# Kernel optimization log

Measured on AMD Instinct MI355X. Metric: run time of the kernel, lower is better.

The kernel has to match this reference:

```python
import jax, jax.numpy as jnp
import numpy as np

EPS = 1e-5

def setup_inputs() -> dict:
    key = jax.random.key(0)
    ks = jax.random.split(key, 4)
    B, C, H, W = 32, 256, 32, 32
    x = jax.random.normal(ks[0], (B, C, H, W), dtype=jnp.float32)
    gamma = jnp.ones((C,), dtype=jnp.float32)
    beta = jnp.zeros((C,), dtype=jnp.float32)
    # torch nn.Linear init scale ~ 1/sqrt(fan_in)
    W_kqv = jax.random.normal(ks[1], (3 * C, C), dtype=jnp.float32) / np.sqrt(C)
    b_kqv = jnp.zeros((3 * C,), dtype=jnp.float32)
    W_proj = jax.random.normal(ks[2], (C, C), dtype=jnp.float32) / np.sqrt(C)
    b_proj = jnp.zeros((C,), dtype=jnp.float32)
    return {"x": x, "gamma": gamma, "beta": beta, "W_kqv": W_kqv,
            "b_kqv": b_kqv, "W_proj": W_proj, "b_proj": b_proj}

def reference(x, gamma, beta, W_kqv, b_kqv, W_proj, b_proj):
    B, C, H, W = x.shape
    scale = jnp.sqrt(jnp.asarray(C, dtype=x.dtype))
    # BatchNorm2d (training-mode batch statistics, biased variance, eps=1e-5)
    mean = jnp.mean(x, axis=(0, 2, 3), keepdims=True)
    var = jnp.var(x, axis=(0, 2, 3), keepdims=True)
    t = (x - mean) * jax.lax.rsqrt(var + EPS)
    t = t * gamma[None, :, None, None] + beta[None, :, None, None]
    # [B, C, H, W] -> [B, N, C] with N = H*W
    t = t.reshape(B, C, H * W).transpose(0, 2, 1)
    kqv = t @ W_kqv.T + b_kqv           # [B, N, 3C]
    q, k, v = jnp.split(kqv, 3, axis=-1)  # each [B, N, C]
    s = jnp.einsum('bnc,bmc->bnm', q, k) / scale  # [B, N, N]
    attn = jax.nn.softmax(s, axis=-1)
    o = jnp.einsum('bnm,bmc->bnc', attn, v)        # [B, N, C]
    o = o @ W_proj.T + b_proj
    o = o.transpose(0, 2, 1).reshape(B, C, H, W)
    return o + x
```

## Files before the change

kernel.cpp:

```cpp
#include <hip/hip_runtime.h>

typedef unsigned short u16;
typedef __attribute__((ext_vector_type(8))) short bf16x8;
typedef __attribute__((ext_vector_type(4))) float f32x4;

__device__ __forceinline__ float bf2f(u16 u) {
  union { unsigned u; float f; } c; c.u = ((unsigned)u) << 16; return c.f;
}
__device__ __forceinline__ u16 f2bf(float f) {
  union { float f; unsigned u; } c; c.f = f;
  unsigned u = c.u;
  return (u16)((u + 0x7FFFu + ((u >> 16) & 1u)) >> 16);
}
__device__ __forceinline__ void gld16(const void* g, void* l) {
  __builtin_amdgcn_global_load_lds(
      (__attribute__((address_space(1))) void*)g,
      (__attribute__((address_space(3))) void*)l, 16, 0, 0);
}

#define SYNCB() do { \
  asm volatile("s_waitcnt vmcnt(0) lgkmcnt(0)" ::: "memory"); \
  __builtin_amdgcn_s_barrier(); \
  __builtin_amdgcn_sched_barrier(0); \
} while (0)

#define BB 32
#define CC 256
#define NN 1024

__global__ __launch_bounds__(256) void convert_w_kernel(
    const float* __restrict__ Wk, const float* __restrict__ bk,
    const float* __restrict__ Wp, const float* __restrict__ bp,
    u16* __restrict__ Wkb, u16* __restrict__ bkb,
    u16* __restrict__ Wpb, u16* __restrict__ bpb)
{
  int b = blockIdx.x, t = threadIdx.x;
  const float* src; u16* dst; int idx, n;
  if (b < 768)       { src = Wk; dst = Wkb; idx = b * 256 + t;        n = 196608; }
  else if (b < 771)  { src = bk; dst = bkb; idx = (b - 768) * 256 + t; n = 768;   }
  else if (b < 1027) { src = Wp; dst = Wpb; idx = (b - 771) * 256 + t; n = 65536; }
  else               { src = bp; dst = bpb; idx = t;                  n = 256;    }
  if (idx < n) dst[idx] = f2bf(src[idx]);
}

__global__ __launch_bounds__(256) void bn_stats_kernel(
    const float* __restrict__ x, const float* __restrict__ gamma,
    const float* __restrict__ beta, float* __restrict__ scl, float* __restrict__ sft)
{
  int c = blockIdx.x;
  int tid = threadIdx.x;
  float s = 0.f, q = 0.f;
  for (int g = tid; g < 8192; g += 256) {
    int b = g >> 8;
    int n = (g & 255) * 4;
    float4 v = *reinterpret_cast<const float4*>(x + (((size_t)(b * CC + c)) << 10) + n);
    s += v.x + v.y + v.z + v.w;
    q += v.x * v.x + v.y * v.y + v.z * v.z + v.w * v.w;
  }
  __shared__ float rs[256], rq[256];
  rs[tid] = s; rq[tid] = q;
  __syncthreads();
  for (int off = 128; off > 0; off >>= 1) {
    if (tid < off) { rs[tid] += rs[tid + off]; rq[tid] += rq[tid + off]; }
    __syncthreads();
  }
  if (tid == 0) {
    float mean = rs[0] * (1.f / 32768.f);
    float var  = rq[0] * (1.f / 32768.f) - mean * mean;
    float rstd = rsqrtf(var + 1e-5f);
    float g = gamma[c] * rstd;
    scl[c] = g;
    sft[c] = beta[c] - mean * g;
  }
}

__global__ __launch_bounds__(256, 2) void qkv_fused_kernel(
    const float* __restrict__ x, const float* __restrict__ scl,
    const float* __restrict__ sft, const u16* __restrict__ Wkb,
    const u16* __restrict__ bkb, u16* __restrict__ qkout, u16* __restrict__ vt)
{
  __shared__ __align__(16) u16 As[2][128 * 32];
  __shared__ __align__(16) u16 Bs[2][256 * 32];
  __shared__ __align__(16) float SS[512];
  int bid = blockIdx.x;
  int bx = bid & 255, by = bid >> 8;
  int b = bx >> 3, nsp0 = (bx & 7) * 128;
  int tid = threadIdx.x, lane = tid & 63, w = tid >> 6;
  int lq = lane & 15, quad = lane >> 4;
  int wm = (w >> 1) * 64, wn = (w & 1) * 128;
  int ar = lane >> 2, ac = (lane & 3) * 8;
  int rbB = w * 64;
  int nn = tid & 127, ci0 = (tid >> 7) * 16;

  const float* xb = x + (((size_t)(b * CC)) << 10) + nsp0 + nn;
  const u16* Bw = Wkb + (size_t)(by * 256) * 256;

  f32x4 zero = {0.f, 0.f, 0.f, 0.f};
  f32x4 acc[4][8];
  #pragma unroll
  for (int i = 0; i < 4; ++i)
    #pragma unroll
    for (int j = 0; j < 8; ++j) acc[i][j] = zero;

  int swz = (nn >> 1) & 3;
  int jj0 = ci0 >> 3;

  if (tid < 128) {
    const float* src = (tid < 64) ? (scl + tid * 4) : (sft + (tid - 64) * 4);
    float4 v = *reinterpret_cast<const float4*>(src);
    *reinterpret_cast<float4*>(&SS[(tid < 64) ? tid * 4 : 256 + (tid - 64) * 4]) = v;
  }
  __syncthreads();

  float xA[16], xB[16];
  #pragma unroll
  for (int i = 0; i < 4; ++i)
    gld16(Bw + (size_t)(rbB + i * 16 + ar) * 256 + ac, &Bs[0][(rbB + i * 16) * 32]);
  #pragma unroll
  for (int i = 0; i < 16; ++i)
    xA[i] = xb[((size_t)(ci0 + i)) << 10];

  auto body = [&](int t, float (&xc)[16], float (&xn)[16]) {
    int k0 = t * 32;
    if (t < 7) {
      int kn = k0 + 32;
      #pragma unroll
      for (int i = 0; i < 4; ++i)
        gld16(Bw + (size_t)(rbB + i * 16 + ar) * 256 + kn + ac,
              &Bs[(t + 1) & 1][(rbB + i * 16) * 32]);
      #pragma unroll
      for (int i = 0; i < 16; ++i)
        xn[i] = xb[((size_t)(kn + ci0 + i)) << 10];
    }
    float sv[16], hv[16];
    #pragma unroll
    for (int g = 0; g < 4; ++g) {
      f32x4 a = *reinterpret_cast<const f32x4*>(&SS[k0 + ci0 + g * 4]);
      f32x4 d = *reinterpret_cast<const f32x4*>(&SS[256 + k0 + ci0 + g * 4]);
      sv[g * 4 + 0] = a[0]; sv[g * 4 + 1] = a[1]; sv[g * 4 + 2] = a[2]; sv[g * 4 + 3] = a[3];
      hv[g * 4 + 0] = d[0]; hv[g * 4 + 1] = d[1]; hv[g * 4 + 2] = d[2]; hv[g * 4 + 3] = d[3];
    }
    if (t < 7) {
      asm volatile("s_waitcnt vmcnt(20)" ::: "memory");
    } else {
      asm volatile("s_waitcnt vmcnt(0)" ::: "memory");
    }
    __builtin_amdgcn_sched_barrier(0);
    u16 av[16];
    #pragma unroll
    for (int i = 0; i < 16; ++i)
      av[i] = f2bf(xc[i] * sv[i] + hv[i]);
    bf16x8 p0, p1;
    #pragma unroll
    for (int i = 0; i < 8; ++i) { p0[i] = (short)av[i]; p1[i] = (short)av[i + 8]; }
    *reinterpret_cast<bf16x8*>(&As[t & 1][nn * 32 + ((jj0 ^ swz) << 3)]) = p0;
    *reinterpret_cast<bf16x8*>(&As[t & 1][nn * 32 + (((jj0 + 1) ^ swz) << 3)]) = p1;
    asm volatile("s_waitcnt lgkmcnt(0)" ::: "memory");
    __builtin_amdgcn_s_barrier();
    __builtin_amdgcn_sched_barrier(0);

    bf16x8 af[4], bfr[8];
    #pragma unroll
    for (int i = 0; i < 4; ++i) {
      int r = wm + i * 16 + lq;
      af[i] = *reinterpret_cast<const bf16x8*>(
          &As[t & 1][r * 32 + ((quad ^ ((r >> 1) & 3)) << 3)]);
    }
    #pragma unroll
    for (int j = 0; j < 8; ++j)
      bfr[j] = *reinterpret_cast<const bf16x8*>(
          &Bs[t & 1][(wn + j * 16 + lq) * 32 + quad * 8]);
    __builtin_amdgcn_s_setprio(1);
    #pragma unroll
    for (int i = 0; i < 4; ++i)
      #pragma unroll
      for (int j = 0; j < 8; ++j)
        acc[i][j] = __builtin_amdgcn_mfma_f32_16x16x32_bf16(af[i], bfr[j], acc[i][j], 0, 0, 0);
    __builtin_amdgcn_s_setprio(0);
    asm volatile("s_waitcnt lgkmcnt(0)" ::: "memory");
    __builtin_amdgcn_s_barrier();
    __builtin_amdgcn_sched_barrier(0);
  };

  #pragma unroll 1
  for (int tt = 0; tt < 4; ++tt) {
    body(2 * tt,     xA, xB);
    body(2 * tt + 1, xB, xA);
  }

  if (by < 2) {
    #pragma unroll
    for (int j = 0; j < 8; ++j) {
      int col = by * 256 + wn + j * 16 + lq;
      float bv = bf2f(bkb[col]);
      #pragma unroll
      for (int i = 0; i < 4; ++i) {
        int m = (b << 10) + nsp0 + wm + i * 16 + quad * 4;
        #pragma unroll
        for (int r = 0; r < 4; ++r)
          qkout[(size_t)(m + r) * 512 + col] = f2bf(acc[i][j][r] + bv);
      }
    }
  } else {
    #pragma unroll
    for (int j = 0; j < 8; ++j) {
      int col = wn + j * 16 + lq;
      float bv = bf2f(bkb[512 + col]);
      #pragma unroll
      for (int i = 0; i < 4; ++i) {
        int n = nsp0 + wm + i * 16 + quad * 4;
        ushort4 o;
        o.x = f2bf(acc[i][j][0] + bv);
        o.y = f2bf(acc[i][j][1] + bv);
        o.z = f2bf(acc[i][j][2] + bv);
        o.w = f2bf(acc[i][j][3] + bv);
        *reinterpret_cast<ushort4*>(&vt[(size_t)b * 262144 + (size_t)col * 1024 + n]) = o;
      }
    }
  }
}

__global__ __launch_bounds__(256) void gemm_nt_kernel(
    const u16* __restrict__ A, int lda, size_t sA,
    const u16* __restrict__ B, int ldb, size_t sB,
    u16* __restrict__ C, int ldc, size_t sC,
    int K, const u16* __restrict__ bias, float scale, int mode,
    const float* __restrict__ xres, float* __restrict__ outf)
{
  __shared__ u16 As[128 * 32];
  __shared__ u16 Bs[128 * 32];
  int tid = threadIdx.x;
  int m0 = blockIdx.x * 128, n0 = blockIdx.y * 128;
  const u16* Ab = A + (size_t)blockIdx.z * sA;
  const u16* Bb = B + (size_t)blockIdx.z * sB;
  u16* Cb = C + (size_t)blockIdx.z * sC;

  int lane = tid & 63, w = tid >> 6;
  int lq = lane & 15, quad = lane >> 4;
  int wm = (w >> 1) * 64, wn = (w & 1) * 64;
  int ar = lane >> 2, ac = (lane & 3) * 8;
  int rb = w * 32;

  f32x4 zero = {0.f, 0.f, 0.f, 0.f};
  f32x4 acc[4][4];
  #pragma unroll
  for (int i = 0; i < 4; ++i)
    #pragma unroll
    for (int j = 0; j < 4; ++j) acc[i][j] = zero;

  for (int k0 = 0; k0 < K; k0 += 32) {
    __syncthreads();
    gld16(Ab + (size_t)(m0 + rb +      ar) * lda + k0 + ac, &As[(rb     ) * 32]);
    gld16(Ab + (size_t)(m0 + rb + 16 + ar) * lda + k0 + ac, &As[(rb + 16) * 32]);
    gld16(Bb + (size_t)(n0 + rb +      ar) * ldb + k0 + ac, &Bs[(rb     ) * 32]);
    gld16(Bb + (size_t)(n0 + rb + 16 + ar) * ldb + k0 + ac, &Bs[(rb + 16) * 32]);
    __syncthreads();
    bf16x8 af[4], bfr[4];
    #pragma unroll
    for (int i = 0; i < 4; ++i) {
      af[i]  = *reinterpret_cast<const bf16x8*>(&As[(wm + i * 16 + lq) * 32 + quad * 8]);
      bfr[i] = *reinterpret_cast<const bf16x8*>(&Bs[(wn + i * 16 + lq) * 32 + quad * 8]);
    }
    #pragma unroll
    for (int i = 0; i < 4; ++i)
      #pragma unroll
      for (int j = 0; j < 4; ++j)
        acc[i][j] = __builtin_amdgcn_mfma_f32_16x16x32_bf16(af[i], bfr[j], acc[i][j], 0, 0, 0);
  }

  #pragma unroll
  for (int j = 0; j < 4; ++j) {
    int col = n0 + wn + j * 16 + lq;
    float bv = bias ? bf2f(bias[col]) : 0.f;
    #pragma unroll
    for (int i = 0; i < 4; ++i) {
      int rbase = m0 + wm + i * 16 + quad * 4;
      if (mode == 2) {
        int b = rbase >> 10, n = rbase & 1023;
        size_t idx = (((size_t)(b * CC + col)) << 10) + n;
        float4 xv = *reinterpret_cast<const float4*>(xres + idx);
        float4 o;
        o.x = acc[i][j][0] * scale + bv + xv.x;
        o.y = acc[i][j][1] * scale + bv + xv.y;
        o.z = acc[i][j][2] * scale + bv + xv.z;
        o.w = acc[i][j][3] * scale + bv + xv.w;
        *reinterpret_cast<float4*>(outf + idx) = o;
      } else {
        #pragma unroll
        for (int r = 0; r < 4; ++r)
          Cb[(size_t)(rbase + r) * ldc + col] = f2bf(acc[i][j][r] * scale + bv);
      }
    }
  }
}

__global__ __launch_bounds__(512, 2) void attn_kernel(
    const u16* __restrict__ qk,
    const u16* __restrict__ vt,
    u16* __restrict__ o)
{
  __shared__ __align__(16) u16 Ks[2][64 * 256];
  __shared__ __align__(16) u16 Vs[2][256 * 64];
  __shared__ __align__(16) u16 Ps[128 * 64];
  float* rs = (float*)Ps;

  int bid = blockIdx.x;
  int b  = (bid & 7) + 8 * ((bid >> 3) & 3);
  int qt = bid >> 5;
  int tid = threadIdx.x, lane = tid & 63, w = tid >> 6;
  int lq = lane & 15, hh = lane >> 4;
  int wr = w & 3;
  bool isQK = w < 4;

  const u16* qb = qk + ((size_t)b << 10) * 512;
  const u16* kb = qb + 256;
  const u16* vb = vt + ((size_t)b << 18);

  auto stageK = [&](int kt, int bufi) {
    #pragma unroll
    for (int i = 0; i < 4; ++i) {
      int slot = i * 512 + tid;
      int r = slot >> 5, c = slot & 31;
      gld16(kb + (size_t)(kt * 64 + r) * 512 + ((c ^ (r & 7)) << 3),
            &Ks[bufi][(i * 512 + (tid & 448)) * 8]);
    }
  };
  auto stageV = [&](int kt, int bufi) {
    #pragma unroll
    for (int i = 0; i < 4; ++i) {
      int slot = i * 512 + tid;
      int n = slot >> 3, c = slot & 7;
      gld16(vb + (size_t)(n << 10) + kt * 64 + ((c ^ (n & 7)) << 3),
            &Vs[bufi][(i * 512 + (tid & 448)) * 8]);
    }
  };

  f32x4 zero = {0.f, 0.f, 0.f, 0.f};

  stageK(0, 0);
  SYNCB();

  if (isQK) {
    int q0 = qt * 128 + wr * 32;
    bf16x8 qf[2][8];
    #pragma unroll
    for (int qi = 0; qi < 2; ++qi)
      #pragma unroll
      for (int kk = 0; kk < 8; ++kk)
        qf[qi][kk] = *reinterpret_cast<const bf16x8*>(
            qb + (size_t)(q0 + qi * 16 + lq) * 512 + kk * 32 + hh * 8);
    float runsum[2][4] = {{0.f, 0.f, 0.f, 0.f}, {0.f, 0.f, 0.f, 0.f}};

    #pragma unroll 1
    for (int p = 0; p <= 16; ++p) {
      if (p <= 15) stageV(p, p & 1);
      if (p <= 14) stageK(p + 1, (p + 1) & 1);
      u16 pbv[2][4][4];
      if (p <= 15) {
        const u16* Kc = Ks[p & 1];
        f32x4 sacc[2][4];
        #pragma unroll
        for (int qi = 0; qi < 2; ++qi)
          #pragma unroll
          for (int ni = 0; ni < 4; ++ni) sacc[qi][ni] = zero;
        #pragma unroll
        for (int kk = 0; kk < 8; ++kk) {
          bf16x8 kf[4];
          #pragma unroll
          for (int ni = 0; ni < 4; ++ni) {
            int r = ni * 16 + lq;
            kf[ni] = *reinterpret_cast<const bf16x8*>(
                &Kc[r * 256 + (((kk * 4 + hh) ^ (r & 7)) << 3)]);
          }
          __builtin_amdgcn_s_setprio(1);
          #pragma unroll
          for (int qi = 0; qi < 2; ++qi)
            #pragma unroll
            for (int ni = 0; ni < 4; ++ni)
              sacc[qi][ni] = __builtin_amdgcn_mfma_f32_16x16x32_bf16(
                  qf[qi][kk], kf[ni], sacc[qi][ni], 0, 0, 0);
          __builtin_amdgcn_s_setprio(0);
        }
        #pragma unroll
        for (int qi = 0; qi < 2; ++qi)
          #pragma unroll
          for (int ni = 0; ni < 4; ++ni)
            #pragma unroll
            for (int rr = 0; rr < 4; ++rr) {
              float pexp = __expf(sacc[qi][ni][rr] * 0.0625f);
              u16 pb = f2bf(pexp);
              runsum[qi][rr] += bf2f(pb);
              pbv[qi][ni][rr] = pb;
            }
      }
      SYNCB();
      if (p <= 15) {
        #pragma unroll
        for (int qi = 0; qi < 2; ++qi)
          #pragma unroll
          for (int ni = 0; ni < 4; ++ni)
            #pragma unroll
            for (int rr = 0; rr < 4; ++rr) {
              int q = wr * 32 + qi * 16 + hh * 4 + rr;
              int kcol = ni * 16 + lq;
              Ps[q * 64 + ((((kcol >> 3) ^ (q & 7)) << 3) | (kcol & 7))] =
                  pbv[qi][ni][rr];
            }
      }
      SYNCB();
    }

    #pragma unroll
    for (int qi = 0; qi < 2; ++qi)
      #pragma unroll
      for (int rr = 0; rr < 4; ++rr) {
        float s = runsum[qi][rr];
        s += __shfl_xor(s, 1, 64);
        s += __shfl_xor(s, 2, 64);
        s += __shfl_xor(s, 4, 64);
        s += __shfl_xor(s, 8, 64);
        if (lq == 0) rs[wr * 32 + qi * 16 + hh * 4 + rr] = 1.f / s;
      }
    SYNCB();
  } else {
    f32x4 oacc[8][4];
    #pragma unroll
    for (int qi = 0; qi < 8; ++qi)
      #pragma unroll
      for (int nj = 0; nj < 4; ++nj) oacc[qi][nj] = zero;

    #pragma unroll 1
    for (int p = 0; p <= 16; ++p) {
      if (p <= 15) stageV(p, p & 1);
      if (p <= 14) stageK(p + 1, (p + 1) & 1);
      if (p >= 1) {
        const u16* Vc = Vs[(p - 1) & 1];
        #pragma unroll
        for (int kk2 = 0; kk2 < 2; ++kk2) {
          bf16x8 pa[8];
          #pragma unroll
          for (int qi = 0; qi < 8; ++qi) {
            int r = qi * 16 + lq;
            pa[qi] = *reinterpret_cast<const bf16x8*>(
                &Ps[r * 64 + (((kk2 * 4 + hh) ^ (r & 7)) << 3)]);
          }
          bf16x8 vf[4];
          #pragma unroll
          for (int nj = 0; nj < 4; ++nj) {
            int n = wr * 64 + nj * 16 + lq;
            vf[nj] = *reinterpret_cast<const bf16x8*>(
                &Vc[n * 64 + (((kk2 * 4 + hh) ^ (n & 7)) << 3)]);
          }
          __builtin_amdgcn_s_setprio(1);
          #pragma unroll
          for (int qi = 0; qi < 8; ++qi)
            #pragma unroll
            for (int nj = 0; nj < 4; ++nj)
              oacc[qi][nj] = __builtin_amdgcn_mfma_f32_16x16x32_bf16(
                  pa[qi], vf[nj], oacc[qi][nj], 0, 0, 0);
          __builtin_amdgcn_s_setprio(0);
        }
      }
      SYNCB();
      SYNCB();
    }

    SYNCB();
    float rinv[8][4];
    #pragma unroll
    for (int qi = 0; qi < 8; ++qi)
      #pragma unroll
      for (int rr = 0; rr < 4; ++rr)
        rinv[qi][rr] = rs[qi * 16 + hh * 4 + rr];
    u16* ob = o + ((size_t)(b << 10) + qt * 128) * 256;
    #pragma unroll
    for (int qi = 0; qi < 8; ++qi)
      #pragma unroll
      for (int nj = 0; nj < 4; ++nj)
        #pragma unroll
        for (int rr = 0; rr < 4; ++rr)
          ob[(size_t)(qi * 16 + hh * 4 + rr) * 256 + wr * 64 + nj * 16 + lq] =
              f2bf(oacc[qi][nj][rr] * rinv[qi][rr]);
  }
}

extern "C" void kernel_launch(void* const* d_in, const int* in_sizes, int n_in,
                              void* d_out, int out_size, void* d_ws, size_t ws_size,
                              hipStream_t stream) {
  const float* x     = (const float*)d_in[0];
  const float* gamma = (const float*)d_in[1];
  const float* beta  = (const float*)d_in[2];
  const float* Wkqv  = (const float*)d_in[3];
  const float* bkqv  = (const float*)d_in[4];
  const float* Wproj = (const float*)d_in[5];
  const float* bproj = (const float*)d_in[6];
  float* out = (float*)d_out;

  char* ws = (char*)d_ws;
  float* scl    = (float*)ws;
  float* sft    = (float*)(ws + 1024);
  u16* Wkb = (u16*)(ws + 4096);
  u16* bkb = Wkb + 196608;
  u16* Wpb = bkb + 768;
  u16* bpb = Wpb + 65536;
  u16* qk   = (u16*)(ws + 1048576);
  u16* vt   = qk + (size_t)32768 * 512;
  u16* o_pv = vt + (size_t)32 * 256 * 1024;

  convert_w_kernel<<<dim3(1028), dim3(256), 0, stream>>>(
      Wkqv, bkqv, Wproj, bproj, Wkb, bkb, Wpb, bpb);
  bn_stats_kernel<<<dim3(256), dim3(256), 0, stream>>>(x, gamma, beta, scl, sft);
  qkv_fused_kernel<<<dim3(768), dim3(256), 0, stream>>>(
      x, scl, sft, Wkb, bkb, qk, vt);
  attn_kernel<<<dim3(256), dim3(512), 0, stream>>>(qk, vt, o_pv);
  gemm_nt_kernel<<<dim3(256, 2, 1), dim3(256), 0, stream>>>(
      o_pv, 256, 0, Wpb, 256, 0, nullptr, 0, 0, 256, bpb, 1.0f, 2, x, out);
}
```

Baseline: 197.4 us.

## Fold BatchNorm affine into QKV weights and vectorize x loads

BatchNorm scale is now folded into the bf16 QKV weight matrix, and the shift is folded into an fp32 bias by a per-row reduction in a new prep kernel that runs after the stats kernel. The QKV GEMM then only converts raw x to bf16, with no per-element FMA and no shared-memory scale/shift table. Its x loads change from 16 scalar loads per stage to 4 float4 loads, with a new LDS swizzle for the transposed tile. Biases are kept in fp32. Cost: one more dependent kernel step before the GEMM, and bf16 rounding is applied to raw x rather than normalized x, which slightly changes precision.

```diff
diff --git a/kernel.cpp b/kernel.cpp
--- a/kernel.cpp
+++ b/kernel.cpp
@@ -27,21 +27,6 @@
 #define BB 32
 #define CC 256
 #define NN 1024
-
-__global__ __launch_bounds__(256) void convert_w_kernel(
-    const float* __restrict__ Wk, const float* __restrict__ bk,
-    const float* __restrict__ Wp, const float* __restrict__ bp,
-    u16* __restrict__ Wkb, u16* __restrict__ bkb,
-    u16* __restrict__ Wpb, u16* __restrict__ bpb)
-{
-  int b = blockIdx.x, t = threadIdx.x;
-  const float* src; u16* dst; int idx, n;
-  if (b < 768)       { src = Wk; dst = Wkb; idx = b * 256 + t;        n = 196608; }
-  else if (b < 771)  { src = bk; dst = bkb; idx = (b - 768) * 256 + t; n = 768;   }
-  else if (b < 1027) { src = Wp; dst = Wpb; idx = (b - 771) * 256 + t; n = 65536; }
-  else               { src = bp; dst = bpb; idx = t;                  n = 256;    }
-  if (idx < n) dst[idx] = f2bf(src[idx]);
-}
 
 __global__ __launch_bounds__(256) void bn_stats_kernel(
     const float* __restrict__ x, const float* __restrict__ gamma,
@@ -74,14 +59,38 @@
   }
 }
 
+__global__ __launch_bounds__(256) void prep_w_kernel(
+    const float* __restrict__ Wk, const float* __restrict__ bk,
+    const float* __restrict__ Wp, const float* __restrict__ bp,
+    const float* __restrict__ scl, const float* __restrict__ sft,
+    u16* __restrict__ Wkb, float* __restrict__ bkbf,
+    u16* __restrict__ Wpb, float* __restrict__ bpbf)
+{
+  int o = blockIdx.x, c = threadIdx.x;
+  __shared__ float red[256];
+  if (o < 768) {
+    float w = Wk[o * 256 + c];
+    Wkb[o * 256 + c] = f2bf(w * scl[c]);
+    red[c] = w * sft[c];
+    __syncthreads();
+    for (int off = 128; off > 0; off >>= 1) {
+      if (c < off) red[c] += red[c + off];
+      __syncthreads();
+    }
+    if (c == 0) bkbf[o] = bk[o] + red[0];
+  } else {
+    int op = o - 768;
+    Wpb[op * 256 + c] = f2bf(Wp[op * 256 + c]);
+    if (c == 0) bpbf[op] = bp[op];
+  }
+}
+
 __global__ __launch_bounds__(256, 2) void qkv_fused_kernel(
-    const float* __restrict__ x, const float* __restrict__ scl,
-    const float* __restrict__ sft, const u16* __restrict__ Wkb,
-    const u16* __restrict__ bkb, u16* __restrict__ qkout, u16* __restrict__ vt)
+    const float* __restrict__ x, const u16* __restrict__ Wkb,
+    const float* __restrict__ bkbf, u16* __restrict__ qkout, u16* __restrict__ vt)
 {
   __shared__ __align__(16) u16 As[2][128 * 32];
   __shared__ __align__(16) u16 Bs[2][256 * 32];
-  __shared__ __align__(16) float SS[512];
   int bid = blockIdx.x;
   int bx = bid & 255, by = bid >> 8;
   int b = bx >> 3, nsp0 = (bx & 7) * 128;
@@ -90,9 +99,11 @@
   int wm = (w >> 1) * 64, wn = (w & 1) * 128;
   int ar = lane >> 2, ac = (lane & 3) * 8;
   int rbB = w * 64;
-  int nn = tid & 127, ci0 = (tid >> 7) * 16;
-
-  const float* xb = x + (((size_t)(b * CC)) << 10) + nsp0 + nn;
+  int nn4 = (tid & 31) * 4;
+  int c8i = tid >> 5;
+  int cg  = c8i * 4;
+
+  const float* xb = x + (((size_t)(b * CC)) << 10) + nsp0 + nn4;
   const u16* Bw = Wkb + (size_t)(by * 256) * 256;
 
   f32x4 zero = {0.f, 0.f, 0.f, 0.f};
@@ -102,25 +113,15 @@
     #pragma unroll
     for (int j = 0; j < 8; ++j) acc[i][j] = zero;
 
-  int swz = (nn >> 1) & 3;
-  int jj0 = ci0 >> 3;
-
-  if (tid < 128) {
-    const float* src = (tid < 64) ? (scl + tid * 4) : (sft + (tid - 64) * 4);
-    float4 v = *reinterpret_cast<const float4*>(src);
-    *reinterpret_cast<float4*>(&SS[(tid < 64) ? tid * 4 : 256 + (tid - 64) * 4]) = v;
-  }
-  __syncthreads();
-
-  float xA[16], xB[16];
+  float4 xA[4], xB[4];
   #pragma unroll
   for (int i = 0; i < 4; ++i)
     gld16(Bw + (size_t)(rbB + i * 16 + ar) * 256 + ac, &Bs[0][(rbB + i * 16) * 32]);
   #pragma unroll
-  for (int i = 0; i < 16; ++i)
-    xA[i] = xb[((size_t)(ci0 + i)) << 10];
-
-  auto body = [&](int t, float (&xc)[16], float (&xn)[16]) {
+  for (int ci = 0; ci < 4; ++ci)
+    xA[ci] = *reinterpret_cast<const float4*>(xb + ((size_t)(cg + ci) << 10));
+
+  auto body = [&](int t, float4 (&xc)[4], float4 (&xn)[4]) {
     int k0 = t * 32;
     if (t < 7) {
       int kn = k0 + 32;
@@ -129,32 +130,33 @@
         gld16(Bw + (size_t)(rbB + i * 16 + ar) * 256 + kn + ac,
               &Bs[(t + 1) & 1][(rbB + i * 16) * 32]);
       #pragma unroll
-      for (int i = 0; i < 16; ++i)
-        xn[i] = xb[((size_t)(kn + ci0 + i)) << 10];
-    }
-    float sv[16], hv[16];
-    #pragma unroll
-    for (int g = 0; g < 4; ++g) {
-      f32x4 a = *reinterpret_cast<const f32x4*>(&SS[k0 + ci0 + g * 4]);
-      f32x4 d = *reinterpret_cast<const f32x4*>(&SS[256 + k0 + ci0 + g * 4]);
-      sv[g * 4 + 0] = a[0]; sv[g * 4 + 1] = a[1]; sv[g * 4 + 2] = a[2]; sv[g * 4 + 3] = a[3];
-      hv[g * 4 + 0] = d[0]; hv[g * 4 + 1] = d[1]; hv[g * 4 + 2] = d[2]; hv[g * 4 + 3] = d[3];
+      for (int ci = 0; ci < 4; ++ci)
+        xn[ci] = *reinterpret_cast<const float4*>(xb + ((size_t)(kn + cg + ci) << 10));
     }
     if (t < 7) {
-      asm volatile("s_waitcnt vmcnt(20)" ::: "memory");
+      asm volatile("s_waitcnt vmcnt(8)" ::: "memory");
     } else {
       asm volatile("s_waitcnt vmcnt(0)" ::: "memory");
     }
     __builtin_amdgcn_sched_barrier(0);
-    u16 av[16];
-    #pragma unroll
-    for (int i = 0; i < 16; ++i)
-      av[i] = f2bf(xc[i] * sv[i] + hv[i]);
-    bf16x8 p0, p1;
-    #pragma unroll
-    for (int i = 0; i < 8; ++i) { p0[i] = (short)av[i]; p1[i] = (short)av[i + 8]; }
-    *reinterpret_cast<bf16x8*>(&As[t & 1][nn * 32 + ((jj0 ^ swz) << 3)]) = p0;
-    *reinterpret_cast<bf16x8*>(&As[t & 1][nn * 32 + (((jj0 + 1) ^ swz) << 3)]) = p1;
+    u16 av[4][4];
+    #pragma unroll
+    for (int ci = 0; ci < 4; ++ci) {
+      av[ci][0] = f2bf(xc[ci].x);
+      av[ci][1] = f2bf(xc[ci].y);
+      av[ci][2] = f2bf(xc[ci].z);
+      av[ci][3] = f2bf(xc[ci].w);
+    }
+    int c16 = c8i >> 1, lo8 = (c8i & 1) * 4;
+    #pragma unroll
+    for (int ni = 0; ni < 4; ++ni) {
+      int n = nn4 + ni;
+      int s2 = (n >> 2) & 3;
+      ushort4 o4;
+      o4.x = av[0][ni]; o4.y = av[1][ni]; o4.z = av[2][ni]; o4.w = av[3][ni];
+      *reinterpret_cast<ushort4*>(
+          &As[t & 1][n * 32 + ((c16 ^ s2) * 8 + lo8)]) = o4;
+    }
     asm volatile("s_waitcnt lgkmcnt(0)" ::: "memory");
     __builtin_amdgcn_s_barrier();
     __builtin_amdgcn_sched_barrier(0);
@@ -164,7 +166,7 @@
     for (int i = 0; i < 4; ++i) {
       int r = wm + i * 16 + lq;
       af[i] = *reinterpret_cast<const bf16x8*>(
-          &As[t & 1][r * 32 + ((quad ^ ((r >> 1) & 3)) << 3)]);
+          &As[t & 1][r * 32 + ((quad ^ ((r >> 2) & 3)) * 8)]);
     }
     #pragma unroll
     for (int j = 0; j < 8; ++j)
@@ -192,7 +194,7 @@
     #pragma unroll
     for (int j = 0; j < 8; ++j) {
       int col = by * 256 + wn + j * 16 + lq;
-      float bv = bf2f(bkb[col]);
+      float bv = bkbf[col];
       #pragma unroll
       for (int i = 0; i < 4; ++i) {
         int m = (b << 10) + nsp0 + wm + i * 16 + quad * 4;
@@ -205,7 +207,7 @@
     #pragma unroll
     for (int j = 0; j < 8; ++j) {
       int col = wn + j * 16 + lq;
-      float bv = bf2f(bkb[512 + col]);
+      float bv = bkbf[512 + col];
       #pragma unroll
       for (int i = 0; i < 4; ++i) {
         int n = nsp0 + wm + i * 16 + quad * 4;
@@ -224,7 +226,7 @@
     const u16* __restrict__ A, int lda, size_t sA,
     const u16* __restrict__ B, int ldb, size_t sB,
     u16* __restrict__ C, int ldc, size_t sC,
-    int K, const u16* __restrict__ bias, float scale, int mode,
+    int K, const float* __restrict__ bias, float scale, int mode,
     const float* __restrict__ xres, float* __restrict__ outf)
 {
   __shared__ u16 As[128 * 32];
@@ -271,7 +273,7 @@
   #pragma unroll
   for (int j = 0; j < 4; ++j) {
     int col = n0 + wn + j * 16 + lq;
-    float bv = bias ? bf2f(bias[col]) : 0.f;
+    float bv = bias ? bias[col] : 0.f;
     #pragma unroll
     for (int i = 0; i < 4; ++i) {
       int rbase = m0 + wm + i * 16 + quad * 4;
@@ -497,22 +499,22 @@
   float* out = (float*)d_out;
 
   char* ws = (char*)d_ws;
-  float* scl    = (float*)ws;
-  float* sft    = (float*)(ws + 1024);
-  u16* Wkb = (u16*)(ws + 4096);
-  u16* bkb = Wkb + 196608;
-  u16* Wpb = bkb + 768;
-  u16* bpb = Wpb + 65536;
+  float* scl  = (float*)ws;
+  float* sft  = (float*)(ws + 1024);
+  u16* Wkb    = (u16*)(ws + 4096);
+  u16* Wpb    = (u16*)(ws + 397312);
+  float* bkbf = (float*)(ws + 528384);
+  float* bpbf = (float*)(ws + 531456);
   u16* qk   = (u16*)(ws + 1048576);
   u16* vt   = qk + (size_t)32768 * 512;
   u16* o_pv = vt + (size_t)32 * 256 * 1024;
 
-  convert_w_kernel<<<dim3(1028), dim3(256), 0, stream>>>(
-      Wkqv, bkqv, Wproj, bproj, Wkb, bkb, Wpb, bpb);
   bn_stats_kernel<<<dim3(256), dim3(256), 0, stream>>>(x, gamma, beta, scl, sft);
+  prep_w_kernel<<<dim3(1024), dim3(256), 0, stream>>>(
+      Wkqv, bkqv, Wproj, bproj, scl, sft, Wkb, bkbf, Wpb, bpbf);
   qkv_fused_kernel<<<dim3(768), dim3(256), 0, stream>>>(
-      x, scl, sft, Wkb, bkb, qk, vt);
+      x, Wkb, bkbf, qk, vt);
   attn_kernel<<<dim3(256), dim3(512), 0, stream>>>(qk, vt, o_pv);
   gemm_nt_kernel<<<dim3(256, 2, 1), dim3(256), 0, stream>>>(
-      o_pv, 256, 0, Wpb, 256, 0, nullptr, 0, 0, 256, bpb, 1.0f, 2, x, out);
-}
+      o_pv, 256, 0, Wpb, 256, 0, nullptr, 0, 0, 256, bpbf, 1.0f, 2, x, out);
+}
```

After: 199.7 us. No clear change (+1.1%).
